# Optimization experiments

Hardware: AMD Instinct MI355X
Metric: run time of the kernel (lower is better)

Reference implementation:

```python
import jax, jax.numpy as jnp
import numpy as np

P = 7       # patch (window) size
H_HEADS = 8
D_HEAD = 64
SCALE = D_HEAD ** -0.5


def setup_inputs() -> dict:
    key = jax.random.key(0)
    k1, k2, k3, k4 = jax.random.split(key, 4)
    dim, inner = 256, H_HEADS * D_HEAD
    fmap = jax.random.normal(k1, (32, 56, 56, dim), dtype=jnp.float32)
    Wq = jax.random.normal(k2, (dim, inner), dtype=jnp.float32) * (dim ** -0.5)
    Wkv = jax.random.normal(k3, (dim, 2 * inner), dtype=jnp.float32) * (dim ** -0.5)
    Wo = jax.random.normal(k4, (inner, dim), dtype=jnp.float32) * (inner ** -0.5)
    bo = jnp.zeros((dim,), dtype=jnp.float32)
    return {"fmap": fmap, "Wq": Wq, "Wkv": Wkv, "Wo": Wo, "bo": bo}


def reference(fmap, Wq, Wkv, Wo, bo):
    b, X, Y, c = fmap.shape
    x, y = X // P, Y // P
    h, d = H_HEADS, D_HEAD
    # window partition: b (x p1) (y p2) c -> (b x y) p1 p2 c
    f = fmap.reshape(b, x, P, y, P, c).transpose(0, 1, 3, 2, 4, 5)
    f = f.reshape(b * x * y, P, P, c)
    # 1x1 convs == matmul over channels
    q = f @ Wq                       # (B, p, p, h*d)
    k_, v = jnp.split(f @ Wkv, 2, axis=-1)
    B = b * x * y
    pp = P * P
    def to_heads(t):  # (B,p,p,h*d) -> (B,h,pp,d)
        return t.reshape(B, pp, h, d).transpose(0, 2, 1, 3)
    q, k_, v = map(to_heads, (q, k_, v))
    dots = jnp.einsum('bhid,bhjd->bhij', q, k_) * SCALE
    attn = jax.nn.softmax(dots, axis=-1)
    out = jnp.einsum('bhij,bhjd->bhid', attn, v)      # (B,h,pp,d)
    # (b x y h) (p1 p2) d -> b (x p1) (y p2) (h d)
    out = out.reshape(b, x, y, h, P, P, d)
    out = out.transpose(0, 1, 4, 2, 5, 3, 6).reshape(b, X, Y, h * d)
    return out @ Wo + bo
```

## Files before the change

kernel.cpp:

```cpp
#include <hip/hip_runtime.h>
#include <hip/hip_bf16.h>

typedef __bf16 bf16;
typedef __bf16 bf16x4 __attribute__((ext_vector_type(4)));
typedef __bf16 bf16x8 __attribute__((ext_vector_type(8)));
typedef float f32x4 __attribute__((ext_vector_type(4)));

#define TOK 100352
#define ATT_SCALE 0.125f

#define GLOAD_LDS16(g, l)                                                        \
  __builtin_amdgcn_global_load_lds((const __attribute__((address_space(1))) void*)(g), \
                                   (__attribute__((address_space(3))) void*)(l), 16, 0, 0)

__global__ __launch_bounds__(256) void transpose_cast_k(const float* __restrict__ in,
                                                        bf16* __restrict__ out, int R, int C) {
  __shared__ float t[32][33];
  int c0 = blockIdx.x * 32, r0 = blockIdx.y * 32;
  int tx = threadIdx.x, ty = threadIdx.y;
#pragma unroll
  for (int i = ty; i < 32; i += 8)
    t[i][tx] = in[(size_t)(r0 + i) * C + c0 + tx];
  __syncthreads();
#pragma unroll
  for (int i = ty; i < 32; i += 8)
    out[(size_t)(c0 + i) * R + r0 + tx] = (bf16)t[tx][i];
}

__global__ __launch_bounds__(256, 2) void qkvg_k(const float* __restrict__ fmap,
                                                 const bf16* __restrict__ Bt,
                                                 bf16* __restrict__ qkv2,
                                                 bf16* __restrict__ Vtg, int wbase0) {
  __shared__ bf16 Bs[128 * 64];
  const int tid = threadIdx.x;
  const int lane = tid & 63, wv = tid >> 6;
  const int l15 = lane & 15, l4 = lane >> 4;
  const int blk = blockIdx.x;
  bf16x8 af[2][8];
  int wl[2], tt[2];
#pragma unroll
  for (int m = 0; m < 2; ++m) {
    int tokl = blk * 128 + wv * 32 + m * 16 + l15;
    int w = tokl / 49, t = tokl - w * 49;
    wl[m] = w; tt[m] = t;
    int wg = wbase0 + w;
    int p1 = t / 7, p2 = t - p1 * 7;
    const float* ab = fmap +
        (size_t)((((wg >> 6) * 56) + ((wg >> 3) & 7) * 7 + p1) * 56 + (wg & 7) * 7 + p2) * 256;
#pragma unroll
    for (int j = 0; j < 8; ++j) {
      const float* p = ab + j * 32 + l4 * 8;
      float4 f0 = *(const float4*)p;
      float4 f1 = *(const float4*)(p + 4);
      bf16x8 o;
      o[0] = (bf16)f0.x; o[1] = (bf16)f0.y; o[2] = (bf16)f0.z; o[3] = (bf16)f0.w;
      o[4] = (bf16)f1.x; o[5] = (bf16)f1.y; o[6] = (bf16)f1.z; o[7] = (bf16)f1.w;
      af[m][j] = o;
    }
  }
  const int sg = lane >> 3;
  const int scol = ((lane & 7) ^ (sg & 7)) * 8;
  for (int bn = 0; bn < 12; ++bn) {
    f32x4 acc[2][8] = {};
    for (int ks = 0; ks < 4; ++ks) {
      __syncthreads();
#pragma unroll
      for (int i = 0; i < 4; ++i)
        GLOAD_LDS16(Bt + (size_t)(bn * 128 + wv * 32 + i * 8 + sg) * 256 + ks * 64 + scol,
                    Bs + wv * 2048 + i * 512);
      __syncthreads();
#pragma unroll
      for (int kk = 0; kk < 2; ++kk) {
        bf16x8 bfr[8];
#pragma unroll
        for (int n = 0; n < 8; ++n) {
          int rv = n * 16 + l15;
          bfr[n] = *(const bf16x8*)((const char*)Bs +
                   ((rv * 128 + kk * 64 + l4 * 16) ^ ((rv & 7) << 4)));
        }
#pragma unroll
        for (int m = 0; m < 2; ++m)
#pragma unroll
          for (int n = 0; n < 8; ++n)
            acc[m][n] =
                __builtin_amdgcn_mfma_f32_16x16x32_bf16(bfr[n], af[m][ks * 2 + kk], acc[m][n], 0, 0, 0);
      }
    }
    if (bn < 8) {
#pragma unroll
      for (int m = 0; m < 2; ++m) {
        size_t row = (size_t)blk * 128 + wv * 32 + m * 16 + l15;
#pragma unroll
        for (int n = 0; n < 8; ++n) {
          bf16x4 pk;
#pragma unroll
          for (int r = 0; r < 4; ++r) pk[r] = (bf16)acc[m][n][r];
          *(bf16x4*)(qkv2 + row * 1024 + bn * 128 + n * 16 + l4 * 4) = pk;
        }
      }
    } else {
#pragma unroll
      for (int m = 0; m < 2; ++m) {
#pragma unroll
        for (int n = 0; n < 8; ++n) {
          int d0 = (bn - 8) * 128 + n * 16 + l4 * 4;
          int h = d0 >> 6, dd = d0 & 63;
          size_t vb = ((size_t)wl[m] * 8 + h) * 4096 + (size_t)dd * 64 + tt[m];
#pragma unroll
          for (int r = 0; r < 4; ++r) Vtg[vb + (size_t)r * 64] = (bf16)acc[m][n][r];
        }
      }
    }
  }
}

__global__ __launch_bounds__(256) void attn2_k(const bf16* __restrict__ qkv2,
                                               const bf16* __restrict__ Vtg,
                                               const bf16* __restrict__ Wo_t,
                                               const float* __restrict__ bias,
                                               float* __restrict__ out, int wbase) {
  __shared__ bf16 Qs[64 * 64], Ks[64 * 64], Vt[64 * 64], Ps[4 * 16 * 64], HO[64 * 64];
  const int w = blockIdx.x;
  const int tid = threadIdx.x, lane = tid & 63, wv = tid >> 6;
  const int l15 = lane & 15, l4 = lane >> 4;
  const size_t bqk = (size_t)w * 49 * 1024;
  const bf16* vbase = Vtg + (size_t)w * 8 * 4096;
  const int wg = wbase + w;
  char* pbase = (char*)Ps + wv * 2048;
  const int sr = wv * 8 + (lane >> 3);
  const int scc = ((lane & 7) ^ ((lane >> 3) & 7)) * 8;
  f32x4 acco[4][4] = {};
  for (int h = 0; h < 8; ++h) {
#pragma unroll
    for (int i = 0; i < 2; ++i) {
      GLOAD_LDS16(qkv2 + bqk + (size_t)(i * 32 + sr) * 1024 + h * 64 + scc,
                  Qs + i * 2048 + wv * 512);
      GLOAD_LDS16(qkv2 + bqk + (size_t)(i * 32 + sr) * 1024 + 512 + h * 64 + scc,
                  Ks + i * 2048 + wv * 512);
      GLOAD_LDS16(vbase + (size_t)h * 4096 + (i * 32 + sr) * 64 + scc,
                  Vt + i * 2048 + wv * 512);
    }
    __syncthreads();
    f32x4 s[4] = {};
#pragma unroll
    for (int kk = 0; kk < 2; ++kk) {
      int rq = wv * 16 + l15;
      bf16x8 aq = *(const bf16x8*)((const char*)Qs +
                  ((rq * 128 + kk * 64 + l4 * 16) ^ ((rq & 7) << 4)));
#pragma unroll
      for (int n = 0; n < 4; ++n) {
        int rk = n * 16 + l15;
        bf16x8 bk = *(const bf16x8*)((const char*)Ks +
                    ((rk * 128 + kk * 64 + l4 * 16) ^ ((rk & 7) << 4)));
        s[n] = __builtin_amdgcn_mfma_f32_16x16x32_bf16(aq, bk, s[n], 0, 0, 0);
      }
    }
    float pr[4][4];
#pragma unroll
    for (int reg = 0; reg < 4; ++reg) {
      float m = -1e30f;
#pragma unroll
      for (int n = 0; n < 4; ++n) {
        float v = s[n][reg] * ATT_SCALE;
        if (n * 16 + l15 < 49) m = fmaxf(m, v);
      }
#pragma unroll
      for (int d = 1; d < 16; d <<= 1) m = fmaxf(m, __shfl_xor(m, d));
      float sum = 0.f;
#pragma unroll
      for (int n = 0; n < 4; ++n) {
        float p = (n * 16 + l15 < 49) ? __expf(s[n][reg] * ATT_SCALE - m) : 0.f;
        pr[n][reg] = p;
        sum += p;
      }
#pragma unroll
      for (int d = 1; d < 16; d <<= 1) sum += __shfl_xor(sum, d);
      float inv = 1.f / sum;
#pragma unroll
      for (int n = 0; n < 4; ++n) pr[n][reg] *= inv;
    }
#pragma unroll
    for (int n = 0; n < 4; ++n)
#pragma unroll
      for (int reg = 0; reg < 4; ++reg) {
        int rl = l4 * 4 + reg, col = n * 16 + l15;
        int off = ((rl * 64 + col) * 2) ^ ((rl & 7) << 4);
        *(bf16*)(pbase + off) = (bf16)pr[n][reg];
      }
    f32x4 o[4] = {};
#pragma unroll
    for (int kk = 0; kk < 2; ++kk) {
      int rp = l15;
      bf16x8 ap = *(const bf16x8*)(pbase +
                  ((rp * 128 + kk * 64 + l4 * 16) ^ ((rp & 7) << 4)));
#pragma unroll
      for (int n = 0; n < 4; ++n) {
        int rv = n * 16 + l15;
        bf16x8 bv = *(const bf16x8*)((const char*)Vt +
                    ((rv * 128 + kk * 64 + l4 * 16) ^ ((rv & 7) << 4)));
        o[n] = __builtin_amdgcn_mfma_f32_16x16x32_bf16(bv, ap, o[n], 0, 0, 0);
      }
    }
    {
      int hrow = wv * 16 + l15;
#pragma unroll
      for (int n = 0; n < 4; ++n) {
        bf16x4 pk;
#pragma unroll
        for (int r = 0; r < 4; ++r) pk[r] = (bf16)o[n][r];
        int off = (hrow * 128 + n * 32 + l4 * 8) ^ ((hrow & 7) << 4);
        *(bf16x4*)((char*)HO + off) = pk;
      }
    }
    __syncthreads();
#pragma unroll
    for (int kk = 0; kk < 2; ++kk) {
      bf16x8 af[4];
#pragma unroll
      for (int m = 0; m < 4; ++m) {
        int r = m * 16 + l15;
        af[m] = *(const bf16x8*)((const char*)HO +
                 ((r * 128 + kk * 64 + l4 * 16) ^ ((r & 7) << 4)));
      }
#pragma unroll
      for (int n = 0; n < 4; ++n) {
        int wr = wv * 64 + n * 16 + l15;
        bf16x8 bv = *(const bf16x8*)(Wo_t + (size_t)wr * 512 + h * 64 + kk * 32 + l4 * 8);
#pragma unroll
        for (int m = 0; m < 4; ++m)
          acco[m][n] = __builtin_amdgcn_mfma_f32_16x16x32_bf16(bv, af[m], acco[m][n], 0, 0, 0);
      }
    }
  }
  int bb = wg >> 6, xx = (wg >> 3) & 7, yy = wg & 7;
#pragma unroll
  for (int m = 0; m < 4; ++m) {
    int rl = m * 16 + l15;
    if (rl < 49) {
      int p1 = rl / 7, p2 = rl - p1 * 7;
      size_t orow = (size_t)(bb * 56 + xx * 7 + p1) * 56 + yy * 7 + p2;
      float* op = out + orow * 256 + wv * 64;
#pragma unroll
      for (int n = 0; n < 4; ++n) {
        int col = n * 16 + l4 * 4;
        float4 b4 = *(const float4*)(bias + wv * 64 + col);
        float4 v;
        v.x = acco[m][n][0] + b4.x;
        v.y = acco[m][n][1] + b4.y;
        v.z = acco[m][n][2] + b4.z;
        v.w = acco[m][n][3] + b4.w;
        *(float4*)(op + col) = v;
      }
    }
  }
}

extern "C" void kernel_launch(void* const* d_in, const int* in_sizes, int n_in,
                              void* d_out, int out_size, void* d_ws, size_t ws_size,
                              hipStream_t stream) {
  const float* fmap = (const float*)d_in[0];
  const float* Wq = (const float*)d_in[1];
  const float* Wkv = (const float*)d_in[2];
  const float* Wo = (const float*)d_in[3];
  const float* bo = (const float*)d_in[4];
  float* out = (float*)d_out;
  char* ws = (char*)d_ws;

  const size_t WQKV_B = 1536ull * 256 * 2;
  const size_t WO_B = 256ull * 512 * 2;
  const size_t wbytes = WQKV_B + WO_B;

  int nc = 0;
  size_t Tc = 0, VtgB = 0;
  for (int c = 2; c <= 16; c <<= 1) {
    size_t tc = TOK / c;
    size_t vb = (tc / 49) * 65536ull;
    if (wbytes + vb + tc * 2048ull + 65536ull <= ws_size) { nc = c; Tc = tc; VtgB = vb; break; }
  }
  if (nc == 0) return;

  bf16* Wqkv_t = (bf16*)(ws);
  bf16* Wo_t = (bf16*)(ws + WQKV_B);
  bf16* Vtg = (bf16*)(ws + wbytes);
  bf16* qkv2 = (bf16*)(ws + wbytes + VtgB);

  hipMemsetAsync(Vtg, 0, VtgB, stream);

  hipLaunchKernelGGL(transpose_cast_k, dim3(16, 8), dim3(32, 8), 0, stream, Wq, Wqkv_t, 256, 512);
  hipLaunchKernelGGL(transpose_cast_k, dim3(32, 8), dim3(32, 8), 0, stream, Wkv,
                     Wqkv_t + 512 * 256, 256, 1024);
  hipLaunchKernelGGL(transpose_cast_k, dim3(8, 16), dim3(32, 8), 0, stream, Wo, Wo_t, 512, 256);

  for (int c = 0; c < nc; ++c) {
    int tok0 = (int)(c * Tc);
    int wloc = (int)(Tc / 49);
    hipLaunchKernelGGL(qkvg_k, dim3((int)(Tc / 128)), dim3(256), 0, stream, fmap, Wqkv_t, qkv2,
                       Vtg, tok0 / 49);
    hipLaunchKernelGGL(attn2_k, dim3(wloc), dim3(256), 0, stream, qkv2, Vtg, Wo_t, bo, out,
                       tok0 / 49);
  }
}
```

Before: 347.2 us.

## Split QKV projection across output groups and double-buffer weight tiles

The QKV projection kernel now launches a 2D grid: each block handles one of three 512-wide output groups (Q, K, V) for a 128-token tile instead of all twelve 128-column tiles. Weight tiles are double-buffered in LDS so the next global-to-LDS load overlaps the current MFMA work, cutting one barrier per step. Occupancy is raised to 4 blocks per CU, and chunking may now use a single chunk when workspace allows. In exchange each fmap activation tile is read and converted three times, and LDS use per block doubles.

New measurement: 610.0 us. +75.7%, slower.

```diff
diff --git a/kernel.cpp b/kernel.cpp
--- a/kernel.cpp
+++ b/kernel.cpp
@@ -27,15 +27,16 @@
     out[(size_t)(c0 + i) * R + r0 + tx] = (bf16)t[tx][i];
 }
 
-__global__ __launch_bounds__(256, 2) void qkvg_k(const float* __restrict__ fmap,
+__global__ __launch_bounds__(256, 4) void qkvg_k(const float* __restrict__ fmap,
                                                  const bf16* __restrict__ Bt,
                                                  bf16* __restrict__ qkv2,
                                                  bf16* __restrict__ Vtg, int wbase0) {
-  __shared__ bf16 Bs[128 * 64];
+  __shared__ bf16 Bs[2][128 * 64];
   const int tid = threadIdx.x;
   const int lane = tid & 63, wv = tid >> 6;
   const int l15 = lane & 15, l4 = lane >> 4;
-  const int blk = blockIdx.x;
+  const int g = blockIdx.x;
+  const int blk = blockIdx.y;
   bf16x8 af[2][8];
   int wl[2], tt[2];
 #pragma unroll
@@ -60,58 +61,72 @@
   }
   const int sg = lane >> 3;
   const int scol = ((lane & 7) ^ (sg & 7)) * 8;
-  for (int bn = 0; bn < 12; ++bn) {
-    f32x4 acc[2][8] = {};
-    for (int ks = 0; ks < 4; ++ks) {
-      __syncthreads();
-#pragma unroll
-      for (int i = 0; i < 4; ++i)
-        GLOAD_LDS16(Bt + (size_t)(bn * 128 + wv * 32 + i * 8 + sg) * 256 + ks * 64 + scol,
-                    Bs + wv * 2048 + i * 512);
-      __syncthreads();
-#pragma unroll
-      for (int kk = 0; kk < 2; ++kk) {
-        bf16x8 bfr[8];
-#pragma unroll
-        for (int n = 0; n < 8; ++n) {
-          int rv = n * 16 + l15;
-          bfr[n] = *(const bf16x8*)((const char*)Bs +
-                   ((rv * 128 + kk * 64 + l4 * 16) ^ ((rv & 7) << 4)));
+#define STAGE_B(tt_, buf_)                                                                   \
+  do {                                                                                       \
+    int bn_ = g * 4 + ((tt_) >> 2), ks_ = (tt_) & 3;                                         \
+    _Pragma("unroll") for (int i_ = 0; i_ < 4; ++i_)                                         \
+        GLOAD_LDS16(Bt + (size_t)(bn_ * 128 + wv * 32 + i_ * 8 + sg) * 256 + ks_ * 64 + scol,\
+                    Bs[buf_] + wv * 2048 + i_ * 512);                                        \
+  } while (0)
+
+  f32x4 acc[2][8] = {};
+  STAGE_B(0, 0);
+  __syncthreads();
+#pragma unroll
+  for (int t = 0; t < 16; ++t) {
+    const int cur = t & 1, ks = t & 3;
+    if (t < 15) STAGE_B(t + 1, cur ^ 1);
+#pragma unroll
+    for (int kk = 0; kk < 2; ++kk) {
+      bf16x8 bfr[8];
+#pragma unroll
+      for (int n = 0; n < 8; ++n) {
+        int rv = n * 16 + l15;
+        bfr[n] = *(const bf16x8*)((const char*)Bs[cur] +
+                 ((rv * 128 + kk * 64 + l4 * 16) ^ ((rv & 7) << 4)));
+      }
+#pragma unroll
+      for (int m = 0; m < 2; ++m)
+#pragma unroll
+        for (int n = 0; n < 8; ++n)
+          acc[m][n] = __builtin_amdgcn_mfma_f32_16x16x32_bf16(bfr[n], af[m][ks * 2 + kk],
+                                                              acc[m][n], 0, 0, 0);
+    }
+    if (ks == 3) {
+      const int bn = g * 4 + (t >> 2);
+      if (g < 2) {
+#pragma unroll
+        for (int m = 0; m < 2; ++m) {
+          size_t row = (size_t)blk * 128 + wv * 32 + m * 16 + l15;
+#pragma unroll
+          for (int n = 0; n < 8; ++n) {
+            bf16x4 pk;
+#pragma unroll
+            for (int r = 0; r < 4; ++r) pk[r] = (bf16)acc[m][n][r];
+            *(bf16x4*)(qkv2 + row * 1024 + bn * 128 + n * 16 + l4 * 4) = pk;
+          }
         }
-#pragma unroll
-        for (int m = 0; m < 2; ++m)
-#pragma unroll
-          for (int n = 0; n < 8; ++n)
-            acc[m][n] =
-                __builtin_amdgcn_mfma_f32_16x16x32_bf16(bfr[n], af[m][ks * 2 + kk], acc[m][n], 0, 0, 0);
-      }
-    }
-    if (bn < 8) {
-#pragma unroll
-      for (int m = 0; m < 2; ++m) {
-        size_t row = (size_t)blk * 128 + wv * 32 + m * 16 + l15;
-#pragma unroll
-        for (int n = 0; n < 8; ++n) {
-          bf16x4 pk;
-#pragma unroll
-          for (int r = 0; r < 4; ++r) pk[r] = (bf16)acc[m][n][r];
-          *(bf16x4*)(qkv2 + row * 1024 + bn * 128 + n * 16 + l4 * 4) = pk;
+      } else {
+#pragma unroll
+        for (int m = 0; m < 2; ++m) {
+#pragma unroll
+          for (int n = 0; n < 8; ++n) {
+            int d0 = (bn - 8) * 128 + n * 16 + l4 * 4;
+            int h = d0 >> 6, dd = d0 & 63;
+            size_t vb = ((size_t)wl[m] * 8 + h) * 4096 + (size_t)dd * 64 + tt[m];
+#pragma unroll
+            for (int r = 0; r < 4; ++r) Vtg[vb + (size_t)r * 64] = (bf16)acc[m][n][r];
+          }
         }
       }
-    } else {
-#pragma unroll
-      for (int m = 0; m < 2; ++m) {
-#pragma unroll
-        for (int n = 0; n < 8; ++n) {
-          int d0 = (bn - 8) * 128 + n * 16 + l4 * 4;
-          int h = d0 >> 6, dd = d0 & 63;
-          size_t vb = ((size_t)wl[m] * 8 + h) * 4096 + (size_t)dd * 64 + tt[m];
-#pragma unroll
-          for (int r = 0; r < 4; ++r) Vtg[vb + (size_t)r * 64] = (bf16)acc[m][n][r];
-        }
-      }
-    }
-  }
+#pragma unroll
+      for (int m = 0; m < 2; ++m)
+#pragma unroll
+        for (int n = 0; n < 8; ++n) acc[m][n] = (f32x4){0.f, 0.f, 0.f, 0.f};
+    }
+    __syncthreads();
+  }
+#undef STAGE_B
 }
 
 __global__ __launch_bounds__(256) void attn2_k(const bf16* __restrict__ qkv2,
@@ -272,7 +287,7 @@
 
   int nc = 0;
   size_t Tc = 0, VtgB = 0;
-  for (int c = 2; c <= 16; c <<= 1) {
+  for (int c = 1; c <= 16; c <<= 1) {
     size_t tc = TOK / c;
     size_t vb = (tc / 49) * 65536ull;
     if (wbytes + vb + tc * 2048ull + 65536ull <= ws_size) { nc = c; Tc = tc; VtgB = vb; break; }
@@ -294,8 +309,8 @@
   for (int c = 0; c < nc; ++c) {
     int tok0 = (int)(c * Tc);
     int wloc = (int)(Tc / 49);
-    hipLaunchKernelGGL(qkvg_k, dim3((int)(Tc / 128)), dim3(256), 0, stream, fmap, Wqkv_t, qkv2,
-                       Vtg, tok0 / 49);
+    hipLaunchKernelGGL(qkvg_k, dim3(3, (int)(Tc / 128)), dim3(256), 0, stream, fmap, Wqkv_t,
+                       qkv2, Vtg, tok0 / 49);
     hipLaunchKernelGGL(attn2_k, dim3(wloc), dim3(256), 0, stream, qkv2, Vtg, Wo_t, bo, out,
                        tok0 / 49);
   }
```
